# Kernel tuning notes

Hardware: AMD Instinct MI355X
Metric: run time of the kernel (lower is better)

## Reference

```python
import jax, jax.numpy as jnp
import numpy as np

N_USERS = 200000
N_ITEMS = 100000
N_NODES = N_USERS + N_ITEMS
N_EDGES = 4800000
EMB = 64
BATCH = 4096


def setup_inputs() -> dict:
    key = jax.random.key(0)
    ks = jax.random.split(key, 7)
    user_id = jax.random.randint(ks[0], (BATCH,), 0, N_USERS, dtype=jnp.int64 if jax.config.jax_enable_x64 else jnp.int32)
    item_id = jax.random.randint(ks[1], (BATCH,), 0, N_ITEMS, dtype=jnp.int64 if jax.config.jax_enable_x64 else jnp.int32)
    adj_row = jax.random.randint(ks[2], (N_EDGES,), 0, N_NODES, dtype=jnp.int32)
    adj_col = jax.random.randint(ks[3], (N_EDGES,), 0, N_NODES, dtype=jnp.int32)
    # normalized adjacency values (positive, ~1/deg scale)
    adj_vals = jax.random.uniform(ks[4], (N_EDGES,), dtype=jnp.float32) * 0.1
    user_emb = jax.random.normal(ks[5], (N_USERS, EMB), dtype=jnp.float32)
    item_emb = jax.random.normal(ks[6], (N_ITEMS, EMB), dtype=jnp.float32)
    return {"user_emb": user_emb, "item_emb": item_emb,
            "adj_row": adj_row, "adj_col": adj_col, "adj_vals": adj_vals,
            "user_id": user_id, "item_id": item_id}


def _spmm(row, col, vals, x):
    # sparse [N,N] @ dense [N,D] via gather + segment_sum
    msg = vals[:, None] * x[col]              # [nnz, D]
    return jax.ops.segment_sum(msg, row, num_segments=N_NODES)


def reference(user_emb, item_emb, adj_row, adj_col, adj_vals, user_id, item_id):
    x0 = jnp.concatenate([user_emb, item_emb], axis=0)   # [N, D] ego embeddings
    # single euler step of dx/dt = A@x + e with e = x0, t: 0 -> 1 (dt = 1):
    # z1 = x0 + (A@x0 + x0) = 2*x0 + A@x0
    ax = _spmm(adj_row, adj_col, adj_vals, x0)
    z1 = 2.0 * x0 + ax
    u_all = z1[:N_USERS]
    i_all = z1[N_USERS:]
    return (u_all[user_id], i_all[item_id])
```

## Files before the change

### kernel.cpp

```cpp
#include <hip/hip_runtime.h>

#define N_USERS 200000
#define N_ITEMS 100000
#define N_NODES 300000
#define N_EDGES 4800000
#define EMB 64
#define BATCH 4096
#define NSLOTS (2 * BATCH)
#define NBITMAP ((N_NODES + 31) / 32)
#define CAP 64

typedef unsigned int u32;

__global__ void k_init(int* __restrict__ node2slot, u32* __restrict__ bitmap,
                       u32* __restrict__ slot_count) {
    int i = blockIdx.x * blockDim.x + threadIdx.x;
    if (i < N_NODES) node2slot[i] = -1;
    if (i < NBITMAP) bitmap[i] = 0u;
    if (i < NSLOTS) slot_count[i] = 0u;
}

__global__ void k_map(const int* __restrict__ user_id, const int* __restrict__ item_id,
                      int* __restrict__ node2slot, u32* __restrict__ bitmap) {
    int b = blockIdx.x * blockDim.x + threadIdx.x;
    if (b >= NSLOTS) return;
    int node = (b < BATCH) ? user_id[b] : (N_USERS + item_id[b - BATCH]);
    atomicCAS(&node2slot[node], -1, b);
    atomicOr(&bitmap[node >> 5], 1u << (node & 31));
}

__global__ void k_filter(const int4* __restrict__ adj_row4, const u32* __restrict__ bitmap,
                         const int* __restrict__ node2slot,
                         u32* __restrict__ slot_count, u32* __restrict__ slot_edges) {
    u32 i = blockIdx.x * blockDim.x + threadIdx.x;
    if (i >= N_EDGES / 4) return;
    int4 rr = adj_row4[i];
    u32 e0 = i * 4u;
    #pragma unroll
    for (int k = 0; k < 4; k++) {
        int r = (&rr.x)[k];
        if ((bitmap[r >> 5] >> (r & 31)) & 1u) {
            int s = node2slot[r];
            u32 p = atomicAdd(&slot_count[s], 1u);
            if (p < CAP) slot_edges[(u32)s * CAP + p] = e0 + (u32)k;
        }
    }
}

__global__ void k_accum(const u32* __restrict__ slot_count, const u32* __restrict__ slot_edges,
                        const int* __restrict__ adj_col, const float* __restrict__ vals,
                        const float* __restrict__ user_emb, const float* __restrict__ item_emb,
                        const int* __restrict__ user_id, const int* __restrict__ item_id,
                        float* __restrict__ out) {
    int lane = threadIdx.x & 63;
    u32 s = (u32)(blockIdx.x * blockDim.x + threadIdx.x) >> 6;
    if (s >= NSLOTS) return;
    u32 cnt = slot_count[s];
    if (cnt > CAP) cnt = CAP;
    int c = 0; float v = 0.f;
    if ((u32)lane < cnt) {
        u32 e = slot_edges[s * CAP + (u32)lane];
        c = adj_col[e];
        v = vals[e];
    }
    float a0 = 0.f, a1 = 0.f;
    u32 j = 0;
    for (; j + 2 <= cnt; j += 2) {
        int c0 = __shfl(c, (int)j);     float v0 = __shfl(v, (int)j);
        int c1 = __shfl(c, (int)j + 1); float v1 = __shfl(v, (int)j + 1);
        const float* x0p = (c0 < N_USERS) ? user_emb + (size_t)c0 * EMB
                                          : item_emb + (size_t)(c0 - N_USERS) * EMB;
        const float* x1p = (c1 < N_USERS) ? user_emb + (size_t)c1 * EMB
                                          : item_emb + (size_t)(c1 - N_USERS) * EMB;
        a0 += v0 * x0p[lane];
        a1 += v1 * x1p[lane];
    }
    if (j < cnt) {
        int c0 = __shfl(c, (int)j); float v0 = __shfl(v, (int)j);
        const float* x0p = (c0 < N_USERS) ? user_emb + (size_t)c0 * EMB
                                          : item_emb + (size_t)(c0 - N_USERS) * EMB;
        a0 += v0 * x0p[lane];
    }
    int node = (s < BATCH) ? user_id[s] : (N_USERS + item_id[s - BATCH]);
    const float* xr = (node < N_USERS) ? user_emb + (size_t)node * EMB
                                       : item_emb + (size_t)(node - N_USERS) * EMB;
    out[(size_t)s * EMB + lane] = 2.f * xr[lane] + (a0 + a1);
}

__global__ void k_dup(const int* __restrict__ user_id, const int* __restrict__ item_id,
                      const int* __restrict__ node2slot, float* __restrict__ out) {
    int t = blockIdx.x * blockDim.x + threadIdx.x;
    int o = t >> 6, lane = t & 63;
    if (o >= NSLOTS) return;
    int node = (o < BATCH) ? user_id[o] : (N_USERS + item_id[o - BATCH]);
    int s = node2slot[node];
    if (s != o) out[(size_t)o * EMB + lane] = out[(size_t)s * EMB + lane];
}

extern "C" void kernel_launch(void* const* d_in, const int* in_sizes, int n_in,
                              void* d_out, int out_size, void* d_ws, size_t ws_size,
                              hipStream_t stream) {
    const float* user_emb = (const float*)d_in[0];
    const float* item_emb = (const float*)d_in[1];
    const int* adj_row = (const int*)d_in[2];
    const int* adj_col = (const int*)d_in[3];
    const float* adj_vals = (const float*)d_in[4];
    const int* user_id = (const int*)d_in[5];
    const int* item_id = (const int*)d_in[6];
    float* out = (float*)d_out;

    char* ws = (char*)d_ws;
    size_t off = 0;
    int* node2slot = (int*)(ws + off);  off += ((size_t)N_NODES * 4 + 255) & ~(size_t)255;
    u32* bitmap    = (u32*)(ws + off);  off += ((size_t)NBITMAP * 4 + 255) & ~(size_t)255;
    u32* slot_count= (u32*)(ws + off);  off += ((size_t)NSLOTS * 4 + 255) & ~(size_t)255;
    u32* slot_edges= (u32*)(ws + off);

    const int B = 256;
    k_init<<<(N_NODES + B - 1) / B, B, 0, stream>>>(node2slot, bitmap, slot_count);
    k_map<<<(NSLOTS + B - 1) / B, B, 0, stream>>>(user_id, item_id, node2slot, bitmap);
    k_filter<<<(N_EDGES / 4 + B - 1) / B, B, 0, stream>>>((const int4*)adj_row, bitmap,
                                                          node2slot, slot_count, slot_edges);
    k_accum<<<(NSLOTS * 64 + B - 1) / B, B, 0, stream>>>(slot_count, slot_edges, adj_col,
                                                         adj_vals, user_emb, item_emb,
                                                         user_id, item_id, out);
    k_dup<<<(NSLOTS * 64 + B - 1) / B, B, 0, stream>>>(user_id, item_id, node2slot, out);
}
```

Before: 175.9 us.

## Drop bitmap and dup kernel, store col/val in buckets, unroll gather by four

Removes the bitmap prefilter and tests node2slot directly in the filter, so each edge costs one 1.2MB-table lookup instead of a bitmap check. The filter now writes (col, val) pairs into the slot buckets, which saves the accumulate kernel an indirect load of adj_col and vals. The accumulate kernel runs per output row, resolves duplicate ids through node2slot, and writes every output directly, so the separate duplicate-copy kernel goes away. The gather loop is unrolled to four accumulators to raise memory-level parallelism, at the cost of redundant gather work for duplicated ids and more random lookups in the filter.

```diff
diff --git a/kernel.cpp b/kernel.cpp
--- a/kernel.cpp
+++ b/kernel.cpp
@@ -7,94 +7,89 @@
 #define EMB 64
 #define BATCH 4096
 #define NSLOTS (2 * BATCH)
-#define NBITMAP ((N_NODES + 31) / 32)
 #define CAP 64
 
 typedef unsigned int u32;
 
-__global__ void k_init(int* __restrict__ node2slot, u32* __restrict__ bitmap,
-                       u32* __restrict__ slot_count) {
+__global__ void k_init(int* __restrict__ node2slot, u32* __restrict__ slot_count) {
     int i = blockIdx.x * blockDim.x + threadIdx.x;
     if (i < N_NODES) node2slot[i] = -1;
-    if (i < NBITMAP) bitmap[i] = 0u;
     if (i < NSLOTS) slot_count[i] = 0u;
 }
 
 __global__ void k_map(const int* __restrict__ user_id, const int* __restrict__ item_id,
-                      int* __restrict__ node2slot, u32* __restrict__ bitmap) {
+                      int* __restrict__ node2slot) {
     int b = blockIdx.x * blockDim.x + threadIdx.x;
     if (b >= NSLOTS) return;
     int node = (b < BATCH) ? user_id[b] : (N_USERS + item_id[b - BATCH]);
     atomicCAS(&node2slot[node], -1, b);
-    atomicOr(&bitmap[node >> 5], 1u << (node & 31));
 }
 
-__global__ void k_filter(const int4* __restrict__ adj_row4, const u32* __restrict__ bitmap,
-                         const int* __restrict__ node2slot,
-                         u32* __restrict__ slot_count, u32* __restrict__ slot_edges) {
+__global__ void k_filter(const int4* __restrict__ adj_row4, const int* __restrict__ adj_col,
+                         const float* __restrict__ vals, const int* __restrict__ node2slot,
+                         u32* __restrict__ slot_count, uint2* __restrict__ bucket) {
     u32 i = blockIdx.x * blockDim.x + threadIdx.x;
     if (i >= N_EDGES / 4) return;
     int4 rr = adj_row4[i];
     u32 e0 = i * 4u;
     #pragma unroll
     for (int k = 0; k < 4; k++) {
-        int r = (&rr.x)[k];
-        if ((bitmap[r >> 5] >> (r & 31)) & 1u) {
-            int s = node2slot[r];
+        int s = node2slot[(&rr.x)[k]];
+        if (s >= 0) {
+            u32 e = e0 + (u32)k;
             u32 p = atomicAdd(&slot_count[s], 1u);
-            if (p < CAP) slot_edges[(u32)s * CAP + p] = e0 + (u32)k;
+            if (p < CAP) {
+                uint2 ent;
+                ent.x = (u32)adj_col[e];
+                ent.y = __float_as_uint(vals[e]);
+                bucket[(u32)s * CAP + p] = ent;
+            }
         }
     }
 }
 
-__global__ void k_accum(const u32* __restrict__ slot_count, const u32* __restrict__ slot_edges,
-                        const int* __restrict__ adj_col, const float* __restrict__ vals,
+__global__ void k_accum(const int* __restrict__ node2slot,
+                        const u32* __restrict__ slot_count, const uint2* __restrict__ bucket,
                         const float* __restrict__ user_emb, const float* __restrict__ item_emb,
                         const int* __restrict__ user_id, const int* __restrict__ item_id,
                         float* __restrict__ out) {
     int lane = threadIdx.x & 63;
-    u32 s = (u32)(blockIdx.x * blockDim.x + threadIdx.x) >> 6;
-    if (s >= NSLOTS) return;
+    u32 o = (u32)(blockIdx.x * blockDim.x + threadIdx.x) >> 6;
+    if (o >= NSLOTS) return;
+    int node = (o < BATCH) ? user_id[o] : (N_USERS + item_id[o - BATCH]);
+    int s = node2slot[node];
     u32 cnt = slot_count[s];
     if (cnt > CAP) cnt = CAP;
     int c = 0; float v = 0.f;
     if ((u32)lane < cnt) {
-        u32 e = slot_edges[s * CAP + (u32)lane];
-        c = adj_col[e];
-        v = vals[e];
+        uint2 ent = bucket[(u32)s * CAP + (u32)lane];
+        c = (int)ent.x;
+        v = __uint_as_float(ent.y);
     }
-    float a0 = 0.f, a1 = 0.f;
+    float a0 = 0.f, a1 = 0.f, a2 = 0.f, a3 = 0.f;
     u32 j = 0;
-    for (; j + 2 <= cnt; j += 2) {
+    for (; j + 4 <= cnt; j += 4) {
         int c0 = __shfl(c, (int)j);     float v0 = __shfl(v, (int)j);
         int c1 = __shfl(c, (int)j + 1); float v1 = __shfl(v, (int)j + 1);
-        const float* x0p = (c0 < N_USERS) ? user_emb + (size_t)c0 * EMB
-                                          : item_emb + (size_t)(c0 - N_USERS) * EMB;
-        const float* x1p = (c1 < N_USERS) ? user_emb + (size_t)c1 * EMB
-                                          : item_emb + (size_t)(c1 - N_USERS) * EMB;
-        a0 += v0 * x0p[lane];
-        a1 += v1 * x1p[lane];
+        int c2 = __shfl(c, (int)j + 2); float v2 = __shfl(v, (int)j + 2);
+        int c3 = __shfl(c, (int)j + 3); float v3 = __shfl(v, (int)j + 3);
+        const float* p0 = (c0 < N_USERS) ? user_emb + (size_t)c0 * EMB : item_emb + (size_t)(c0 - N_USERS) * EMB;
+        const float* p1 = (c1 < N_USERS) ? user_emb + (size_t)c1 * EMB : item_emb + (size_t)(c1 - N_USERS) * EMB;
+        const float* p2 = (c2 < N_USERS) ? user_emb + (size_t)c2 * EMB : item_emb + (size_t)(c2 - N_USERS) * EMB;
+        const float* p3 = (c3 < N_USERS) ? user_emb + (size_t)c3 * EMB : item_emb + (size_t)(c3 - N_USERS) * EMB;
+        a0 += v0 * p0[lane];
+        a1 += v1 * p1[lane];
+        a2 += v2 * p2[lane];
+        a3 += v3 * p3[lane];
     }
-    if (j < cnt) {
+    for (; j < cnt; j++) {
         int c0 = __shfl(c, (int)j); float v0 = __shfl(v, (int)j);
-        const float* x0p = (c0 < N_USERS) ? user_emb + (size_t)c0 * EMB
-                                          : item_emb + (size_t)(c0 - N_USERS) * EMB;
-        a0 += v0 * x0p[lane];
+        const float* p0 = (c0 < N_USERS) ? user_emb + (size_t)c0 * EMB : item_emb + (size_t)(c0 - N_USERS) * EMB;
+        a0 += v0 * p0[lane];
     }
-    int node = (s < BATCH) ? user_id[s] : (N_USERS + item_id[s - BATCH]);
     const float* xr = (node < N_USERS) ? user_emb + (size_t)node * EMB
                                        : item_emb + (size_t)(node - N_USERS) * EMB;
-    out[(size_t)s * EMB + lane] = 2.f * xr[lane] + (a0 + a1);
-}
-
-__global__ void k_dup(const int* __restrict__ user_id, const int* __restrict__ item_id,
-                      const int* __restrict__ node2slot, float* __restrict__ out) {
-    int t = blockIdx.x * blockDim.x + threadIdx.x;
-    int o = t >> 6, lane = t & 63;
-    if (o >= NSLOTS) return;
-    int node = (o < BATCH) ? user_id[o] : (N_USERS + item_id[o - BATCH]);
-    int s = node2slot[node];
-    if (s != o) out[(size_t)o * EMB + lane] = out[(size_t)s * EMB + lane];
+    out[(size_t)o * EMB + lane] = 2.f * xr[lane] + ((a0 + a1) + (a2 + a3));
 }
 
 extern "C" void kernel_launch(void* const* d_in, const int* in_sizes, int n_in,
@@ -111,18 +106,17 @@
 
     char* ws = (char*)d_ws;
     size_t off = 0;
-    int* node2slot = (int*)(ws + off);  off += ((size_t)N_NODES * 4 + 255) & ~(size_t)255;
-    u32* bitmap    = (u32*)(ws + off);  off += ((size_t)NBITMAP * 4 + 255) & ~(size_t)255;
-    u32* slot_count= (u32*)(ws + off);  off += ((size_t)NSLOTS * 4 + 255) & ~(size_t)255;
-    u32* slot_edges= (u32*)(ws + off);
+    int* node2slot  = (int*)(ws + off);  off += ((size_t)N_NODES * 4 + 255) & ~(size_t)255;
+    u32* slot_count = (u32*)(ws + off);  off += ((size_t)NSLOTS * 4 + 255) & ~(size_t)255;
+    uint2* bucket   = (uint2*)(ws + off);
 
     const int B = 256;
-    k_init<<<(N_NODES + B - 1) / B, B, 0, stream>>>(node2slot, bitmap, slot_count);
-    k_map<<<(NSLOTS + B - 1) / B, B, 0, stream>>>(user_id, item_id, node2slot, bitmap);
-    k_filter<<<(N_EDGES / 4 + B - 1) / B, B, 0, stream>>>((const int4*)adj_row, bitmap,
-                                                          node2slot, slot_count, slot_edges);
-    k_accum<<<(NSLOTS * 64 + B - 1) / B, B, 0, stream>>>(slot_count, slot_edges, adj_col,
-                                                         adj_vals, user_emb, item_emb,
+    k_init<<<(N_NODES + B - 1) / B, B, 0, stream>>>(node2slot, slot_count);
+    k_map<<<(NSLOTS + B - 1) / B, B, 0, stream>>>(user_id, item_id, node2slot);
+    k_filter<<<(N_EDGES / 4 + B - 1) / B, B, 0, stream>>>((const int4*)adj_row, adj_col,
+                                                          adj_vals, node2slot,
+                                                          slot_count, bucket);
+    k_accum<<<(NSLOTS * 64 + B - 1) / B, B, 0, stream>>>(node2slot, slot_count, bucket,
+                                                         user_emb, item_emb,
                                                          user_id, item_id, out);
-    k_dup<<<(NSLOTS * 64 + B - 1) / B, B, 0, stream>>>(user_id, item_id, node2slot, out);
 }
```

Result: slower. 183.5 us (+4.3%).
